# Kernel optimization log

Hardware: AMD Instinct MI355X
Metric: run time of the kernel (lower is better)

Reference implementation:

```python
import jax, jax.numpy as jnp
import numpy as np

D_MODEL = 1024
N_HEADS = 16
D_K = D_MODEL // N_HEADS
D_FF = 4096
EPS = 1e-5


def setup_inputs() -> dict:
    key = jax.random.key(0)
    ks = jax.random.split(key, 12)
    s = 1.0 / np.sqrt(D_MODEL)
    inp = {
        "x": jax.random.normal(ks[0], (2, 2048, D_MODEL), dtype=jnp.float32),
        "Wq": jax.random.normal(ks[1], (D_MODEL, D_MODEL), dtype=jnp.float32) * s,
        "Wk": jax.random.normal(ks[2], (D_MODEL, D_MODEL), dtype=jnp.float32) * s,
        "Wv": jax.random.normal(ks[3], (D_MODEL, D_MODEL), dtype=jnp.float32) * s,
        "Wo": jax.random.normal(ks[4], (D_MODEL, D_MODEL), dtype=jnp.float32) * s,
        "ln1_g": jnp.ones((D_MODEL,), jnp.float32),
        "ln1_b": jnp.zeros((D_MODEL,), jnp.float32),
        "ln2_g": jnp.ones((D_MODEL,), jnp.float32),
        "ln2_b": jnp.zeros((D_MODEL,), jnp.float32),
        "W1": jax.random.normal(ks[5], (D_MODEL, D_FF), dtype=jnp.float32) * s,
        "b1": jnp.zeros((D_FF,), jnp.float32),
        "W2": jax.random.normal(ks[6], (D_FF, D_MODEL), dtype=jnp.float32) * (1.0 / np.sqrt(D_FF)),
        "b2": jnp.zeros((D_MODEL,), jnp.float32),
    }
    return inp


def _layernorm(x, g, b):
    mu = jnp.mean(x, axis=-1, keepdims=True)
    var = jnp.mean(jnp.square(x - mu), axis=-1, keepdims=True)
    return (x - mu) / jnp.sqrt(var + EPS) * g + b


def _mha(x, Wq, Wk, Wv, Wo):
    B, S, D = x.shape
    def split_heads(t):
        return t.reshape(B, S, N_HEADS, D_K).transpose(0, 2, 1, 3)  # [B,H,S,Dk]
    Q = split_heads(x @ Wq)
    K = split_heads(x @ Wk)
    V = split_heads(x @ Wv)
    scores = jnp.einsum("bhsd,bhtd->bhst", Q, K) / np.sqrt(D_K)
    causal = jnp.tril(jnp.ones((S, S), dtype=bool))
    scores = jnp.where(causal, scores, -jnp.inf)
    weights = jax.nn.softmax(scores, axis=-1)
    out = jnp.einsum("bhst,bhtd->bhsd", weights, V)
    out = out.transpose(0, 2, 1, 3).reshape(B, S, D)
    return out @ Wo


def reference(x, Wq, Wk, Wv, Wo, ln1_g, ln1_b, ln2_g, ln2_b, W1, b1, W2, b2):
    # Pre-LN transformer block, dropout in eval mode (identity)
    x = x + _mha(_layernorm(x, ln1_g, ln1_b), Wq, Wk, Wv, Wo)
    h = _layernorm(x, ln2_g, ln2_b)
    ff = jax.nn.gelu(h @ W1 + b1, approximate=False) @ W2 + b2
    return x + ff
```

## Files before the change

kernel.cpp:

```cpp
#include <hip/hip_runtime.h>
#include <cstdint>
#include <cstddef>

#define DEV __device__ __forceinline__

typedef __attribute__((ext_vector_type(8))) __bf16 bf16x8;
typedef __attribute__((ext_vector_type(4))) float f32x4;
typedef __attribute__((ext_vector_type(8))) unsigned short u16x8;

typedef const __attribute__((address_space(1))) void gld_gv;
typedef __attribute__((address_space(3))) void gld_sv;

static constexpr int SEQ = 2048, BAT = 2, DM = 1024, DFF = 4096;
static constexpr int MT = BAT * SEQ;
static constexpr float LOG2E = 1.44269504088896340736f;

DEV unsigned short f2bf_bits(float f) {
    uint32_t u = __builtin_bit_cast(uint32_t, f);
    return (unsigned short)((u + 0x7FFFu + ((u >> 16) & 1u)) >> 16);
}

DEV void gload16(const void* g, void* s) {
    __builtin_amdgcn_global_load_lds((gld_gv*)g, (gld_sv*)s, 16, 0, 0);
}

__global__ __launch_bounds__(256) void wtrans_kernel(const float* __restrict__ W,
        unsigned short* __restrict__ WT, int K, int N, float scale)
{
    __shared__ float tile[64][65];
    const int k0 = blockIdx.x * 64, n0 = blockIdx.y * 64;
    const int t = threadIdx.x, r = t >> 6, c = t & 63;
    #pragma unroll
    for (int p = 0; p < 16; ++p)
        tile[p * 4 + r][c] = W[(size_t)(k0 + p * 4 + r) * N + n0 + c];
    __syncthreads();
    #pragma unroll
    for (int p = 0; p < 16; ++p)
        WT[(size_t)(n0 + p * 4 + r) * K + k0 + c] = f2bf_bits(tile[c][p * 4 + r] * scale);
}

__global__ __launch_bounds__(256) void ln_kernel(const float* __restrict__ x,
        const float* __restrict__ gw, const float* __restrict__ bw,
        unsigned short* __restrict__ y)
{
    const int row = blockIdx.x, t = threadIdx.x;
    const float* xr = x + (size_t)row * DM;
    float4 v = *(const float4*)(xr + t * 4);
    float s = v.x + v.y + v.z + v.w;
    float q = v.x * v.x + v.y * v.y + v.z * v.z + v.w * v.w;
    #pragma unroll
    for (int m = 1; m < 64; m <<= 1) { s += __shfl_xor(s, m); q += __shfl_xor(q, m); }
    __shared__ float red[8];
    const int w = t >> 6;
    if ((t & 63) == 0) { red[w] = s; red[4 + w] = q; }
    __syncthreads();
    s = red[0] + red[1] + red[2] + red[3];
    q = red[4] + red[5] + red[6] + red[7];
    const float mu = s * (1.0f / DM);
    const float rstd = rsqrtf(q * (1.0f / DM) - mu * mu + 1e-5f);
    float4 g4 = *(const float4*)(gw + t * 4);
    float4 b4 = *(const float4*)(bw + t * 4);
    short4 o;
    o.x = (short)f2bf_bits((v.x - mu) * rstd * g4.x + b4.x);
    o.y = (short)f2bf_bits((v.y - mu) * rstd * g4.y + b4.y);
    o.z = (short)f2bf_bits((v.z - mu) * rstd * g4.z + b4.z);
    o.w = (short)f2bf_bits((v.w - mu) * rstd * g4.w + b4.w);
    *(short4*)(y + (size_t)row * DM + t * 4) = o;
}

template<int EPI, int BM, int BN, int WVM, int WVN>
__global__ __launch_bounds__(WVM * WVN * 64, (BN == 64 ? 3 : 2)) void gemm_pipe(
    const unsigned short* __restrict__ A, const unsigned short* __restrict__ BT,
    void* __restrict__ Cp, const float* __restrict__ bias,
    const float* __restrict__ res, int Nsz, int Ksz, float scale)
{
    constexpr int NT = WVM * WVN * 64;
    constexpr int TOTCH = (BM + BN) * 8;
    constexpr int TL = TOTCH / NT;
    constexpr int MREP = BM / (WVM * 16);
    constexpr int WMR = MREP * 16;
    __shared__ alignas(16) unsigned short lds[2][(BM + BN) * 64];

    const int t = threadIdx.x, l = t & 63, w = t >> 6;
    const int wm = w / WVN, wn = w % WVN;
    const int lr = l & 15, lg = l >> 4;
    const int bm = blockIdx.x, bn = blockIdx.y;

    f32x4 acc[MREP][4] = {};

    const int nk = Ksz / 64;

    auto STAGE = [&](int tile, char* slot) {
        const int k0 = tile * 64;
        #pragma unroll
        for (int p = 0; p < TL; ++p) {
            const int ci = t + p * NT;
            const bool isA = ci < BM * 8;
            const int rr = (isA ? ci : ci - BM * 8) >> 3;
            const int cc = ci & 7;
            const unsigned short* srow = isA
                ? A + (size_t)(bm * BM + rr) * Ksz
                : BT + (size_t)(bn * BN + rr) * Ksz;
            gload16(srow + k0 + ((cc ^ (rr & 7)) << 3), slot + ci * 16);
        }
    };

    STAGE(0, (char*)lds[0]);
    STAGE(1, (char*)lds[1]);

    for (int kt = 0; kt < nk; ++kt) {
        char* slot = (char*)lds[kt & 1];
        const char* la = slot;
        const char* lb = slot + BM * 128;
        if (kt + 1 < nk) {
            if constexpr (TL == 8) asm volatile("s_waitcnt vmcnt(8)" ::: "memory");
            else                   asm volatile("s_waitcnt vmcnt(6)" ::: "memory");
        } else {
            asm volatile("s_waitcnt vmcnt(0)" ::: "memory");
        }
        __builtin_amdgcn_s_barrier();
        __builtin_amdgcn_sched_barrier(0);

        __builtin_amdgcn_s_setprio(1);
        #pragma unroll
        for (int ks = 0; ks < 2; ++ks) {
            bf16x8 af[MREP], bfr[4];
            #pragma unroll
            for (int i = 0; i < MREP; ++i) {
                const int ra = wm * WMR + i * 16 + lr;
                af[i] = *(const bf16x8*)(la + (ra * 8 + ((ks * 4 + lg) ^ (ra & 7))) * 16);
            }
            #pragma unroll
            for (int i = 0; i < 4; ++i) {
                const int rb_ = wn * 64 + i * 16 + lr;
                bfr[i] = *(const bf16x8*)(lb + (rb_ * 8 + ((ks * 4 + lg) ^ (rb_ & 7))) * 16);
            }
            #pragma unroll
            for (int mb = 0; mb < MREP; ++mb)
                #pragma unroll
                for (int nb = 0; nb < 4; ++nb) {
                    if (EPI == 4)
                        acc[mb][nb] = __builtin_amdgcn_mfma_f32_16x16x32_bf16(
                            bfr[nb], af[mb], acc[mb][nb], 0, 0, 0);
                    else
                        acc[mb][nb] = __builtin_amdgcn_mfma_f32_16x16x32_bf16(
                            af[mb], bfr[nb], acc[mb][nb], 0, 0, 0);
                }
        }
        __builtin_amdgcn_s_setprio(0);
        __builtin_amdgcn_s_barrier();
        if (kt + 2 < nk) STAGE(kt + 2, slot);
    }

    const int rb = bm * BM + wm * WMR, cb = bn * BN + wn * 64;
    #pragma unroll
    for (int mb = 0; mb < MREP; ++mb)
        #pragma unroll
        for (int nb = 0; nb < 4; ++nb)
            #pragma unroll
            for (int r = 0; r < 4; ++r) {
                float v = acc[mb][nb][r];
                if (EPI == 4) {
                    const int xrow = rb + mb * 16 + lr;
                    const int feat = cb + nb * 16 + lg * 4 + r;
                    const int bb = xrow >> 11, s = xrow & (SEQ - 1);
                    ((unsigned short*)Cp)[((size_t)bb * DM + feat) * SEQ + s] = f2bf_bits(v);
                    continue;
                }
                const int row = rb + mb * 16 + lg * 4 + r;
                const int col = cb + nb * 16 + lr;
                const size_t idx = (size_t)row * Nsz + col;
                if (EPI == 0) {
                    ((unsigned short*)Cp)[idx] = f2bf_bits(v * scale);
                } else if (EPI == 1) {
                    ((float*)Cp)[idx] = v + res[idx];
                } else if (EPI == 2) {
                    float xx = v + bias[col];
                    ((unsigned short*)Cp)[idx] =
                        f2bf_bits(0.5f * xx * (1.0f + erff(xx * 0.70710678118654752f)));
                } else {
                    ((float*)Cp)[idx] = v + bias[col] + res[idx];
                }
            }
}

template<int P>
DEV void phase8_mfma(const char* base, int wm, int lr, int lg,
                     const bf16x8 (&bfr)[2][4], f32x4 (&acc)[8][4]) {
    bf16x8 af[2][2];
    #pragma unroll
    for (int ks = 0; ks < 2; ++ks)
        #pragma unroll
        for (int m = 0; m < 2; ++m) {
            const int ra = wm * 128 + P * 32 + m * 16 + lr;
            af[ks][m] = *(const bf16x8*)(base + (ra * 8 + ((ks * 4 + lg) ^ (ra & 7))) * 16);
        }
    __builtin_amdgcn_s_barrier();
    __builtin_amdgcn_s_setprio(1);
    #pragma unroll
    for (int ks = 0; ks < 2; ++ks)
        #pragma unroll
        for (int m = 0; m < 2; ++m)
            #pragma unroll
            for (int nb = 0; nb < 4; ++nb)
                acc[P * 2 + m][nb] = __builtin_amdgcn_mfma_f32_16x16x32_bf16(
                    af[ks][m], bfr[ks][nb], acc[P * 2 + m][nb], 0, 0, 0);
    __builtin_amdgcn_s_setprio(0);
}

template<int EPI>
__global__ __launch_bounds__(512, 2) void gemm_8ph(
    const unsigned short* __restrict__ A, const unsigned short* __restrict__ BT,
    void* __restrict__ Cp, const float* __restrict__ bias,
    const float* __restrict__ res, int Nsz, int Ksz, float scale)
{
    __shared__ alignas(16) unsigned short lds[2][32768];
    const int t = threadIdx.x, l = t & 63, w = t >> 6;
    const int wm = w >> 2, wn = w & 3;
    const int lr = l & 15, lg = l >> 4;
    const int bm = blockIdx.x, bn = blockIdx.y;

    f32x4 acc[8][4] = {};
    const int nk = Ksz / 64;

    const unsigned short* Ab = A + (size_t)(bm * 256) * Ksz;
    const unsigned short* Bb = BT + (size_t)(bn * 256) * Ksz;

    auto stage = [&](int tile, int region) {
        char* base = (char*)lds[tile & 1];
        const int k0 = tile * 64;
        #pragma unroll
        for (int j = 0; j < 2; ++j) {
            const int ci = t + j * 512;
            const int rr = ci >> 3, c = ci & 7;
            int row; const unsigned short* src; int dchunk;
            if (region == 0)      { row = rr;                          src = Bb; dchunk = 2048 + row * 8 + c; }
            else if (region == 1) { row = 128 + rr;                    src = Bb; dchunk = 2048 + row * 8 + c; }
            else if (region == 2) { row = (rr < 64 ? rr : rr + 64);    src = Ab; dchunk = row * 8 + c; }
            else                  { row = 64 + (rr < 64 ? rr : rr + 64); src = Ab; dchunk = row * 8 + c; }
            gload16(src + (size_t)row * Ksz + k0 + ((c ^ (row & 7)) << 3),
                    base + dchunk * 16);
        }
    };

    stage(0, 0); stage(0, 1); stage(0, 2); stage(0, 3);
    stage(1, 0); stage(1, 1); stage(1, 2);
    asm volatile("s_waitcnt vmcnt(6)" ::: "memory");
    __builtin_amdgcn_s_barrier();
    __builtin_amdgcn_sched_barrier(0);

    bf16x8 bfr[2][4];
    for (int kt = 0; kt < nk; ++kt) {
        const char* base = (const char*)lds[kt & 1];
        if (kt + 1 < nk) stage(kt + 1, 3);
        #pragma unroll
        for (int ks = 0; ks < 2; ++ks)
            #pragma unroll
            for (int nb = 0; nb < 4; ++nb) {
                const int rb_ = wn * 64 + nb * 16 + lr;
                bfr[ks][nb] = *(const bf16x8*)(base
                    + (2048 + rb_ * 8 + ((ks * 4 + lg) ^ (rb_ & 7))) * 16);
            }
        phase8_mfma<0>(base, wm, lr, lg, bfr, acc);
        __builtin_amdgcn_s_barrier();
        if (kt + 2 < nk) stage(kt + 2, 0);
        phase8_mfma<1>(base, wm, lr, lg, bfr, acc);
        __builtin_amdgcn_s_barrier();
        if (kt + 2 < nk) stage(kt + 2, 1);
        phase8_mfma<2>(base, wm, lr, lg, bfr, acc);
        __builtin_amdgcn_s_barrier();
        if (kt + 2 < nk) stage(kt + 2, 2);
        phase8_mfma<3>(base, wm, lr, lg, bfr, acc);
        if (kt + 2 < nk) asm volatile("s_waitcnt vmcnt(6)" ::: "memory");
        else             asm volatile("s_waitcnt vmcnt(0)" ::: "memory");
        __builtin_amdgcn_s_barrier();
        __builtin_amdgcn_sched_barrier(0);
    }

    const int rb = bm * 256 + wm * 128, cb = bn * 256 + wn * 64;
    #pragma unroll
    for (int mb = 0; mb < 8; ++mb)
        #pragma unroll
        for (int nb = 0; nb < 4; ++nb)
            #pragma unroll
            for (int r = 0; r < 4; ++r) {
                float v = acc[mb][nb][r];
                const int row = rb + mb * 16 + lg * 4 + r;
                const int col = cb + nb * 16 + lr;
                const size_t idx = (size_t)row * Nsz + col;
                if (EPI == 2) {
                    float xx = v + bias[col];
                    ((unsigned short*)Cp)[idx] =
                        f2bf_bits(0.5f * xx * (1.0f + erff(xx * 0.70710678118654752f)));
                } else if (EPI == 0) {
                    ((unsigned short*)Cp)[idx] = f2bf_bits(v * scale);
                } else {
                    ((float*)Cp)[idx] = v + bias[col] + res[idx];
                }
            }
}

__global__ __launch_bounds__(512, 2) void attn_kernel(
    const unsigned short* __restrict__ QKg, const unsigned short* __restrict__ VTg,
    unsigned short* __restrict__ Og)
{
    __shared__ alignas(16) unsigned short ldsK[2][128 * 64];
    __shared__ alignas(16) unsigned short ldsVT[2][64 * 128];
    const int t = threadIdx.x, l = t & 63, w = t >> 6;
    const int lr = l & 15, lg = l >> 4;
    const int qtA = blockIdx.x, qtB = 15 - qtA;
    const int bh = blockIdx.y;
    const int b = bh >> 4, h = bh & 15;
    const unsigned short* Qbase = QKg + (size_t)b * SEQ * 2048 + h * 64;
    const unsigned short* Kbase = Qbase + 1024;
    const unsigned short* Vbase = VTg + (size_t)b * DM * SEQ + (size_t)(h * 64) * SEQ;

    const int wq0A = qtA * 128 + w * 16, qrowA = wq0A + lr;
    const int wq0B = qtB * 128 + w * 16, qrowB = wq0B + lr;
    bf16x8 qfA[2], qfB[2];
    #pragma unroll
    for (int ks = 0; ks < 2; ++ks) {
        qfA[ks] = *(const bf16x8*)(Qbase + (size_t)qrowA * 2048 + ks * 32 + lg * 8);
        qfB[ks] = *(const bf16x8*)(Qbase + (size_t)qrowB * 2048 + ks * 32 + lg * 8);
    }

    float m_runA = -1e30f, l_partA = 0.0f;
    float m_runB = -1e30f, l_partB = 0.0f;
    f32x4 oaccA[4] = {}, oaccB[4] = {};

    const int kci[2] = { t, t + 512 };
    const int nkt = qtB + 1;

    #pragma unroll
    for (int p = 0; p < 2; ++p) {
        const int ci = kci[p];
        const int kr = ci >> 3, kc = (ci & 7) ^ (kr & 7);
        gload16(Kbase + (size_t)kr * 2048 + kc * 8, (char*)ldsK[0] + ci * 16);
        const int vr = ci >> 4, vc = (ci & 15) ^ (vr & 15);
        gload16(Vbase + (size_t)vr * SEQ + vc * 8, (char*)ldsVT[0] + ci * 16);
    }
    asm volatile("s_waitcnt vmcnt(0)" ::: "memory");
    __builtin_amdgcn_s_barrier();

    for (int kt = 0; kt < nkt; ++kt) {
        const int cur = kt & 1;
        if (kt + 1 < nkt) {
            #pragma unroll
            for (int p = 0; p < 2; ++p) {
                const int ci = kci[p];
                const int kr = ci >> 3, kc = (ci & 7) ^ (kr & 7);
                gload16(Kbase + (size_t)((kt + 1) * 128 + kr) * 2048 + kc * 8,
                        (char*)ldsK[cur ^ 1] + ci * 16);
                const int vr = ci >> 4, vc = (ci & 15) ^ (vr & 15);
                gload16(Vbase + (size_t)vr * SEQ + (kt + 1) * 128 + vc * 8,
                        (char*)ldsVT[cur ^ 1] + ci * 16);
            }
        }
        const char* lk = (const char*)ldsK[cur];
        const char* lv = (const char*)ldsVT[cur];

        auto process = [&](const bf16x8 (&qf)[2], f32x4 (&oacc)[4],
                           float& m_run, float& l_part, int qrow, bool diag) {
            __builtin_amdgcn_s_setprio(1);
            f32x4 st[8] = {};
            #pragma unroll
            for (int ks = 0; ks < 2; ++ks)
                #pragma unroll
                for (int mb = 0; mb < 8; ++mb) {
                    bf16x8 kf = *(const bf16x8*)(lk + (mb * 16 + lr) * 128
                                                 + (((ks * 4 + lg) ^ (lr & 7)) * 16));
                    st[mb] = __builtin_amdgcn_mfma_f32_16x16x32_bf16(kf, qf[ks], st[mb], 0, 0, 0);
                }
            __builtin_amdgcn_s_setprio(0);

            const int kt0 = kt * 128;
            if (diag) {
                #pragma unroll
                for (int mb = 0; mb < 8; ++mb)
                    #pragma unroll
                    for (int r = 0; r < 4; ++r)
                        if (kt0 + mb * 16 + lg * 4 + r > qrow) st[mb][r] = -1e30f;
            }

            f32x4 mx4 = st[0];
            #pragma unroll
            for (int mb = 1; mb < 8; ++mb) {
                mx4[0] = fmaxf(mx4[0], st[mb][0]); mx4[1] = fmaxf(mx4[1], st[mb][1]);
                mx4[2] = fmaxf(mx4[2], st[mb][2]); mx4[3] = fmaxf(mx4[3], st[mb][3]);
            }
            const float mt = fmaxf(fmaxf(mx4[0], mx4[1]), fmaxf(mx4[2], mx4[3]));

            if (!__all(mt <= m_run + 8.0f)) {
                float mr = fmaxf(mt, __shfl_xor(mt, 16));
                mr = fmaxf(mr, __shfl_xor(mr, 32));
                const float m_new = fmaxf(m_run, mr);
                const float alpha = exp2f((m_run - m_new) * LOG2E);
                l_part *= alpha;
                #pragma unroll
                for (int j = 0; j < 4; ++j) {
                    const float aj = __shfl(alpha, lg * 4 + j);
                    #pragma unroll
                    for (int nb = 0; nb < 4; ++nb) oacc[nb][j] *= aj;
                }
                m_run = m_new;
            }

            const float nml = m_run * LOG2E;
            float rsl = 0.0f;
            #pragma unroll
            for (int mb = 0; mb < 8; ++mb)
                #pragma unroll
                for (int r = 0; r < 4; ++r) {
                    const float p = exp2f(fmaf(st[mb][r], LOG2E, -nml));
                    st[mb][r] = p;
                    rsl += p;
                }
            l_part += rsl;

            bf16x8 pa[4];
            #pragma unroll
            for (int ks = 0; ks < 4; ++ks)
                #pragma unroll
                for (int j = 0; j < 4; ++j) {
                    pa[ks][j]     = (__bf16)st[2 * ks][j];
                    pa[ks][j + 4] = (__bf16)st[2 * ks + 1][j];
                }

            __builtin_amdgcn_s_setprio(1);
            #pragma unroll
            for (int ks = 0; ks < 4; ++ks)
                #pragma unroll
                for (int nb = 0; nb < 4; ++nb) {
                    const int n = nb * 16 + lr;
                    union { bf16x8 v; uint64_t d[2]; } vb;
                    vb.d[0] = *(const uint64_t*)(lv + n * 256
                                + (((4 * ks + (lg >> 1)) ^ (n & 15)) * 16) + 8 * (lg & 1));
                    vb.d[1] = *(const uint64_t*)(lv + n * 256
                                + (((4 * ks + 2 + (lg >> 1)) ^ (n & 15)) * 16) + 8 * (lg & 1));
                    oacc[nb] = __builtin_amdgcn_mfma_f32_16x16x32_bf16(pa[ks], vb.v, oacc[nb], 0, 0, 0);
                }
            __builtin_amdgcn_s_setprio(0);
        };

        if (kt <= qtA) process(qfA, oaccA, m_runA, l_partA, qrowA, kt == qtA);
        process(qfB, oaccB, m_runB, l_partB, qrowB, kt == qtB);

        asm volatile("s_waitcnt vmcnt(0)" ::: "memory");
        __builtin_amdgcn_s_barrier();
    }

    unsigned short* Obase = Og + (size_t)b * SEQ * DM + h * 64;
    {
        float lr_ = l_partA;
        lr_ += __shfl_xor(lr_, 16); lr_ += __shfl_xor(lr_, 32);
        #pragma unroll
        for (int j = 0; j < 4; ++j) {
            const float inv = 1.0f / __shfl(lr_, lg * 4 + j);
            const int row = wq0A + lg * 4 + j;
            #pragma unroll
            for (int nb = 0; nb < 4; ++nb)
                Obase[(size_t)row * DM + nb * 16 + lr] = f2bf_bits(oaccA[nb][j] * inv);
        }
    }
    {
        float lr_ = l_partB;
        lr_ += __shfl_xor(lr_, 16); lr_ += __shfl_xor(lr_, 32);
        #pragma unroll
        for (int j = 0; j < 4; ++j) {
            const float inv = 1.0f / __shfl(lr_, lg * 4 + j);
            const int row = wq0B + lg * 4 + j;
            #pragma unroll
            for (int nb = 0; nb < 4; ++nb)
                Obase[(size_t)row * DM + nb * 16 + lr] = f2bf_bits(oaccB[nb][j] * inv);
        }
    }
}

extern "C" void kernel_launch(void* const* d_in, const int* in_sizes, int n_in,
                              void* d_out, int out_size, void* d_ws, size_t ws_size,
                              hipStream_t stream) {
    (void)in_sizes; (void)n_in; (void)out_size; (void)ws_size;
    const float* x    = (const float*)d_in[0];
    const float* Wq   = (const float*)d_in[1];
    const float* Wk   = (const float*)d_in[2];
    const float* Wv   = (const float*)d_in[3];
    const float* Wo   = (const float*)d_in[4];
    const float* ln1g = (const float*)d_in[5];
    const float* ln1b = (const float*)d_in[6];
    const float* ln2g = (const float*)d_in[7];
    const float* ln2b = (const float*)d_in[8];
    const float* W1   = (const float*)d_in[9];
    const float* b1   = (const float*)d_in[10];
    const float* W2   = (const float*)d_in[11];
    const float* b2   = (const float*)d_in[12];
    float* out = (float*)d_out;

    char* ws = (char*)d_ws;
    const size_t MB = 1ull << 20;
    unsigned short* xn1   = (unsigned short*)(ws + 0 * MB);
    unsigned short* QKb   = (unsigned short*)(ws + 8 * MB);
    unsigned short* VTg   = (unsigned short*)(ws + 24 * MB);
    unsigned short* ffa   = (unsigned short*)(ws + 0 * MB);
    unsigned short* attno = (unsigned short*)(ws + 32 * MB);
    float*          x2    = (float*)(ws + 40 * MB);
    unsigned short* h2    = (unsigned short*)(ws + 56 * MB);
    unsigned short* WqkT  = (unsigned short*)(ws + 64 * MB);
    unsigned short* WvT   = (unsigned short*)(ws + 68 * MB);
    unsigned short* WoT   = (unsigned short*)(ws + 70 * MB);
    unsigned short* W1T   = (unsigned short*)(ws + 72 * MB);
    unsigned short* W2T   = (unsigned short*)(ws + 80 * MB);

    dim3 blk(256);
    wtrans_kernel<<<dim3(16, 16), blk, 0, stream>>>(Wq, WqkT, DM, DM, 0.125f);
    wtrans_kernel<<<dim3(16, 16), blk, 0, stream>>>(Wk, WqkT + DM * DM, DM, DM, 1.0f);
    wtrans_kernel<<<dim3(16, 16), blk, 0, stream>>>(Wv, WvT, DM, DM, 1.0f);
    wtrans_kernel<<<dim3(16, 16), blk, 0, stream>>>(Wo, WoT, DM, DM, 1.0f);
    wtrans_kernel<<<dim3(16, 64), blk, 0, stream>>>(W1, W1T, DM, DFF, 1.0f);
    wtrans_kernel<<<dim3(64, 16), blk, 0, stream>>>(W2, W2T, DFF, DM, 1.0f);

    ln_kernel<<<dim3(MT), blk, 0, stream>>>(x, ln1g, ln1b, xn1);

    gemm_pipe<0, 128, 256, 2, 4><<<dim3(32, 8), dim3(512), 0, stream>>>(
        xn1, WqkT, QKb, nullptr, nullptr, 2048, DM, 1.0f);
    gemm_pipe<4, 128, 64, 4, 1><<<dim3(32, 16), blk, 0, stream>>>(
        xn1, WvT, VTg, nullptr, nullptr, DM, DM, 1.0f);

    attn_kernel<<<dim3(8, 32), dim3(512), 0, stream>>>(QKb, VTg, attno);

    gemm_pipe<1, 128, 64, 4, 1><<<dim3(32, 16), blk, 0, stream>>>(
        attno, WoT, x2, nullptr, x, DM, DM, 1.0f);

    ln_kernel<<<dim3(MT), blk, 0, stream>>>(x2, ln2g, ln2b, h2);

    gemm_8ph<2><<<dim3(16, 16), dim3(512), 0, stream>>>(
        h2, W1T, ffa, b1, nullptr, DFF, DM, 1.0f);
    gemm_pipe<3, 128, 64, 4, 1><<<dim3(32, 16), blk, 0, stream>>>(
        ffa, W2T, out, b2, x2, DM, DFF, 1.0f);
}
```

Before: 241.1 us.

## Interleave both query tiles per K/V fragment load; use tanh-approx GELU

The attention loop now processes query tiles A and B together. Each K and V fragment read from LDS feeds both tiles' MFMAs instead of being reloaded, and the two softmaxes sit between the two matmul phases, with a compile-time branch for iterations where tile A is inactive. This halves LDS fragment reads and gives the scheduler more independent MFMA work, at the cost of higher register pressure. Separately, the FFN GELU epilogue replaces erff with the tanh approximation written as a sigmoid via exp2 and a fast reciprocal, which changes numerics slightly.

```diff
diff --git a/kernel.cpp b/kernel.cpp
--- a/kernel.cpp
+++ b/kernel.cpp
@@ -14,6 +14,9 @@
 static constexpr int SEQ = 2048, BAT = 2, DM = 1024, DFF = 4096;
 static constexpr int MT = BAT * SEQ;
 static constexpr float LOG2E = 1.44269504088896340736f;
+
+struct TrueC  { static constexpr bool value = true;  };
+struct FalseC { static constexpr bool value = false; };
 
 DEV unsigned short f2bf_bits(float f) {
     uint32_t u = __builtin_bit_cast(uint32_t, f);
@@ -289,9 +292,12 @@
                 const int col = cb + nb * 16 + lr;
                 const size_t idx = (size_t)row * Nsz + col;
                 if (EPI == 2) {
-                    float xx = v + bias[col];
+                    const float xx = v + bias[col];
+                    const float tq = xx * xx;
+                    const float u = xx * fmaf(tq, 0.044715f, 1.0f);
+                    const float e = exp2f(u * -2.30220795f);
                     ((unsigned short*)Cp)[idx] =
-                        f2bf_bits(0.5f * xx * (1.0f + erff(xx * 0.70710678118654752f)));
+                        f2bf_bits(xx * __builtin_amdgcn_rcpf(1.0f + e));
                 } else if (EPI == 0) {
                     ((unsigned short*)Cp)[idx] = f2bf_bits(v * scale);
                 } else {
@@ -358,22 +364,10 @@
         }
         const char* lk = (const char*)ldsK[cur];
         const char* lv = (const char*)ldsVT[cur];
-
-        auto process = [&](const bf16x8 (&qf)[2], f32x4 (&oacc)[4],
-                           float& m_run, float& l_part, int qrow, bool diag) {
-            __builtin_amdgcn_s_setprio(1);
-            f32x4 st[8] = {};
-            #pragma unroll
-            for (int ks = 0; ks < 2; ++ks)
-                #pragma unroll
-                for (int mb = 0; mb < 8; ++mb) {
-                    bf16x8 kf = *(const bf16x8*)(lk + (mb * 16 + lr) * 128
-                                                 + (((ks * 4 + lg) ^ (lr & 7)) * 16));
-                    st[mb] = __builtin_amdgcn_mfma_f32_16x16x32_bf16(kf, qf[ks], st[mb], 0, 0, 0);
-                }
-            __builtin_amdgcn_s_setprio(0);
-
-            const int kt0 = kt * 128;
+        const int kt0 = kt * 128;
+
+        auto run_softmax = [&](f32x4 (&st)[8], f32x4 (&oacc)[4], float& m_run,
+                               float& l_part, int qrow, bool diag, bf16x8 (&pa)[4]) {
             if (diag) {
                 #pragma unroll
                 for (int mb = 0; mb < 8; ++mb)
@@ -381,7 +375,6 @@
                     for (int r = 0; r < 4; ++r)
                         if (kt0 + mb * 16 + lg * 4 + r > qrow) st[mb][r] = -1e30f;
             }
-
             f32x4 mx4 = st[0];
             #pragma unroll
             for (int mb = 1; mb < 8; ++mb) {
@@ -389,7 +382,6 @@
                 mx4[2] = fmaxf(mx4[2], st[mb][2]); mx4[3] = fmaxf(mx4[3], st[mb][3]);
             }
             const float mt = fmaxf(fmaxf(mx4[0], mx4[1]), fmaxf(mx4[2], mx4[3]));
-
             if (!__all(mt <= m_run + 8.0f)) {
                 float mr = fmaxf(mt, __shfl_xor(mt, 16));
                 mr = fmaxf(mr, __shfl_xor(mr, 32));
@@ -404,7 +396,6 @@
                 }
                 m_run = m_new;
             }
-
             const float nml = m_run * LOG2E;
             float rsl = 0.0f;
             #pragma unroll
@@ -416,8 +407,6 @@
                     rsl += p;
                 }
             l_part += rsl;
-
-            bf16x8 pa[4];
             #pragma unroll
             for (int ks = 0; ks < 4; ++ks)
                 #pragma unroll
@@ -425,6 +414,28 @@
                     pa[ks][j]     = (__bf16)st[2 * ks][j];
                     pa[ks][j + 4] = (__bf16)st[2 * ks + 1][j];
                 }
+        };
+
+        auto iter_body = [&](auto DOA) {
+            constexpr bool doA = DOA.value;
+            f32x4 stA[8] = {}, stB[8] = {};
+            __builtin_amdgcn_s_setprio(1);
+            #pragma unroll
+            for (int ks = 0; ks < 2; ++ks)
+                #pragma unroll
+                for (int mb = 0; mb < 8; ++mb) {
+                    bf16x8 kf = *(const bf16x8*)(lk + (mb * 16 + lr) * 128
+                                                 + (((ks * 4 + lg) ^ (lr & 7)) * 16));
+                    if constexpr (doA)
+                        stA[mb] = __builtin_amdgcn_mfma_f32_16x16x32_bf16(kf, qfA[ks], stA[mb], 0, 0, 0);
+                    stB[mb] = __builtin_amdgcn_mfma_f32_16x16x32_bf16(kf, qfB[ks], stB[mb], 0, 0, 0);
+                }
+            __builtin_amdgcn_s_setprio(0);
+
+            bf16x8 paA[4], paB[4];
+            if constexpr (doA)
+                run_softmax(stA, oaccA, m_runA, l_partA, qrowA, kt == qtA, paA);
+            run_softmax(stB, oaccB, m_runB, l_partB, qrowB, kt == qtB, paB);
 
             __builtin_amdgcn_s_setprio(1);
             #pragma unroll
@@ -437,13 +448,14 @@
                                 + (((4 * ks + (lg >> 1)) ^ (n & 15)) * 16) + 8 * (lg & 1));
                     vb.d[1] = *(const uint64_t*)(lv + n * 256
                                 + (((4 * ks + 2 + (lg >> 1)) ^ (n & 15)) * 16) + 8 * (lg & 1));
-                    oacc[nb] = __builtin_amdgcn_mfma_f32_16x16x32_bf16(pa[ks], vb.v, oacc[nb], 0, 0, 0);
+                    if constexpr (doA)
+                        oaccA[nb] = __builtin_amdgcn_mfma_f32_16x16x32_bf16(paA[ks], vb.v, oaccA[nb], 0, 0, 0);
+                    oaccB[nb] = __builtin_amdgcn_mfma_f32_16x16x32_bf16(paB[ks], vb.v, oaccB[nb], 0, 0, 0);
                 }
             __builtin_amdgcn_s_setprio(0);
         };
 
-        if (kt <= qtA) process(qfA, oaccA, m_runA, l_partA, qrowA, kt == qtA);
-        process(qfB, oaccB, m_runB, l_partB, qrowB, kt == qtB);
+        if (kt <= qtA) iter_body(TrueC{}); else iter_body(FalseC{});
 
         asm volatile("s_waitcnt vmcnt(0)" ::: "memory");
         __builtin_amdgcn_s_barrier();
```

Result: faster. 230.3 us (-4.5%).
